# Optimization experiments

Measured on AMD Instinct MI355X. Metric: run time of the kernel, lower is better.

## Reference

```python
import jax, jax.numpy as jnp
import numpy as np

N = 50000      # total batched graph nodes (both ASTs of all examples)
E = 30000      # edges per edge type
T = 8          # num edge types (no master node, no sibling edges)
H = 128        # gnn hidden = change_vector_dim // 2
TAG = 32       # change-tag embed size
CONTENT = H - TAG
VOCAB = 20000  # rows of token/content encoding table
B = 64         # num examples
STEPS = (3, 3) # layer_time_steps


def setup_inputs() -> dict:
    key = jax.random.key(0)
    ks = jax.random.split(key, 22)
    s = 0.05
    inp = {}
    inp["node_content_ids"] = jax.random.randint(ks[0], (N,), 0, VOCAB)
    inp["node_tag_ids"] = jax.random.randint(ks[1], (N,), 0, 4)
    inp["edge_src"] = jax.random.randint(ks[2], (T, E), 0, N)
    inp["edge_tgt"] = jax.random.randint(ks[3], (T, E), 0, N)
    inp["node2example"] = jnp.sort(jax.random.randint(ks[4], (N,), 0, B))
    inp["content_table"] = jax.random.normal(ks[5], (VOCAB, CONTENT)) * s
    inp["tag_embedding"] = jax.random.normal(ks[6], (4, TAG)) * s
    inp["msg_W"] = jax.random.normal(ks[7], (2, T, H, H)) * s
    inp["msg_b"] = jax.random.normal(ks[8], (2, T, H)) * s
    inp["gru0_Wih"] = jax.random.normal(ks[9], (H, 3 * H)) * s
    inp["gru0_Whh"] = jax.random.normal(ks[10], (H, 3 * H)) * s
    inp["gru0_bih"] = jax.random.normal(ks[11], (3 * H,)) * s
    inp["gru0_bhh"] = jax.random.normal(ks[12], (3 * H,)) * s
    inp["gru1_Wih"] = jax.random.normal(ks[13], (2 * H, 3 * H)) * s  # layer 1 gets residual concat -> 2H input
    inp["gru1_Whh"] = jax.random.normal(ks[14], (H, 3 * H)) * s
    inp["gru1_bih"] = jax.random.normal(ks[15], (3 * H,)) * s
    inp["gru1_bhh"] = jax.random.normal(ks[16], (3 * H,)) * s
    inp["r1_w"] = jax.random.normal(ks[17], (H,)) * s
    inp["r1_b"] = jax.random.normal(ks[18], ()) * s
    inp["r2_w"] = jax.random.normal(ks[19], (H,)) * s
    inp["r2_b"] = jax.random.normal(ks[20], ()) * s
    return inp


def _gru(x, h, Wih, Whh, bih, bhh):
    # PyTorch GRUCell gate order: r, z, n
    gi = x @ Wih + bih
    gh = h @ Whh + bhh
    i_r, i_z, i_n = jnp.split(gi, 3, axis=-1)
    h_r, h_z, h_n = jnp.split(gh, 3, axis=-1)
    r = jax.nn.sigmoid(i_r + h_r)
    z = jax.nn.sigmoid(i_z + h_z)
    n = jnp.tanh(i_n + r * h_n)
    return (1.0 - z) * n + z * h


def reference(node_content_ids, node_tag_ids, edge_src, edge_tgt, node2example,
              content_table, tag_embedding, msg_W, msg_b,
              gru0_Wih, gru0_Whh, gru0_bih, gru0_bhh,
              gru1_Wih, gru1_Whh, gru1_bih, gru1_bhh,
              r1_w, r1_b, r2_w, r2_b):
    # init node embeddings: [token/content encoding || change-tag embedding] -> [N, H]
    init = jnp.concatenate([content_table[node_content_ids],
                            tag_embedding[node_tag_ids]], axis=-1)
    states = init
    layer_out = []
    for layer, steps in enumerate(STEPS):
        for _ in range(steps):
            src_states = states[edge_src]                                   # [T,E,H] gather
            msgs = jnp.einsum('teh,thd->ted', src_states, msg_W[layer]) \
                   + msg_b[layer][:, None, :]                               # per-edge-type linear
            agg = jnp.zeros_like(states).at[edge_tgt].add(msgs)             # scatter-add to targets
            if layer == 1:
                # residual_connections={1:[0]}: concat initial states with incoming messages
                x = jnp.concatenate([init, agg], axis=-1)
                states = _gru(x, states, gru1_Wih, gru1_Whh, gru1_bih, gru1_bhh)
            else:
                states = _gru(agg, states, gru0_Wih, gru0_Whh, gru0_bih, gru0_bhh)
        layer_out.append(states)
    s1, s2 = layer_out
    # gated scalar readout per layer, pooled per example, concatenated -> [B, 2H]
    g1 = jax.nn.sigmoid(s1 @ r1_w + r1_b)[:, None]
    g2 = jax.nn.sigmoid(s2 @ r2_w + r2_b)[:, None]
    pooled1 = jax.ops.segment_sum(g1 * s1, node2example, num_segments=B)
    pooled2 = jax.ops.segment_sum(g2 * s2, node2example, num_segments=B)
    return jnp.concatenate([pooled1, pooled2], axis=-1)
```

## Files before the change

kernel.cpp:

```cpp
#include <hip/hip_runtime.h>
#include <hip/hip_bf16.h>

#define NN 50000
#define NE 30000
#define NT 8
#define HH 128
#define NB 64
#define CONT 96
#define TPB 16
#define EDGES (NT * NE)
#define SBLK 512
#define SNB ((NN + SBLK - 1) / SBLK)
#define RCH 8
#define NTILE (NN / 16)
#define NPAIR ((NTILE + 1) / 2)
#define XB ((NPAIR + 3) / 4)
#define GGRID ((((XB + 7) / 8)) * 32)

typedef __attribute__((ext_vector_type(8))) short short8;
typedef __attribute__((ext_vector_type(4))) float f32x4;

__device__ __forceinline__ float sigm(float x) { return 1.f / (1.f + __expf(-x)); }
__device__ __forceinline__ float tanhf_fast(float x) {
  float e = __expf(2.f * x);
  return 1.f - 2.f / (e + 1.f);
}
__device__ __forceinline__ unsigned short bfbits(float x) {
  __hip_bfloat16 b = __float2bfloat16(x);
  return *(unsigned short*)&b;
}

__global__ __launch_bounds__(256) void init_kernel(
    const int* __restrict__ cid, const int* __restrict__ tg,
    const float* __restrict__ ctab, const float* __restrict__ ttab,
    __hip_bfloat16* __restrict__ sbf, __hip_bfloat16* __restrict__ ibf)
{
  int i = blockIdx.x * 256 + threadIdx.x;
  if (i >= NN * HH) return;
  int n = i >> 7, d = i & 127;
  float v;
  if (d < CONT) v = ctab[(size_t)cid[n] * CONT + d];
  else          v = ttab[(size_t)tg[n] * 32 + (d - CONT)];
  __hip_bfloat16 b = __float2bfloat16(v);
  sbf[i] = b;
  ibf[i] = b;
}

__global__ __launch_bounds__(256) void hist_kernel(
    const int* __restrict__ etgt, int* __restrict__ cnt)
{
  int i = blockIdx.x * 256 + threadIdx.x;
  if (i >= EDGES) return;
  atomicAdd(&cnt[etgt[i]], 1);
}

__global__ __launch_bounds__(SBLK) void scanA_kernel(
    const int* __restrict__ cnt, int* __restrict__ row_ptr, int* __restrict__ bsum)
{
  __shared__ int sm[SBLK];
  const int tid = threadIdx.x;
  const int i = blockIdx.x * SBLK + tid;
  int v = (i < NN) ? cnt[i] : 0;
  sm[tid] = v;
  __syncthreads();
  for (int off = 1; off < SBLK; off <<= 1) {
    int t = (tid >= off) ? sm[tid - off] : 0;
    __syncthreads();
    sm[tid] += t;
    __syncthreads();
  }
  if (i < NN) row_ptr[i] = sm[tid] - v;
  if (tid == SBLK - 1) bsum[blockIdx.x] = sm[tid];
}

__global__ __launch_bounds__(128) void scanB_kernel(
    const int* __restrict__ bsum, int* __restrict__ boff, int* __restrict__ row_ptr,
    const int* __restrict__ n2e, int* __restrict__ ebnd)
{
  __shared__ int sm[128];
  const int tid = threadIdx.x;
  int v = (tid < SNB) ? bsum[tid] : 0;
  sm[tid] = v;
  __syncthreads();
  for (int off = 1; off < 128; off <<= 1) {
    int t = (tid >= off) ? sm[tid - off] : 0;
    __syncthreads();
    sm[tid] += t;
    __syncthreads();
  }
  if (tid < SNB) boff[tid] = sm[tid] - v;
  if (tid == 127) row_ptr[NN] = sm[127];
  if (tid <= NB) {
    int lo = 0, hi = NN;
    while (lo < hi) { int mid = (lo + hi) >> 1; if (n2e[mid] < tid) lo = mid + 1; else hi = mid; }
    ebnd[tid] = lo;
  }
}

__global__ __launch_bounds__(SBLK) void scanC_kernel(
    int* __restrict__ row_ptr, int* __restrict__ cnt2, const int* __restrict__ boff)
{
  int i = blockIdx.x * SBLK + threadIdx.x;
  if (i >= NN) return;
  int r = row_ptr[i] + boff[blockIdx.x];
  row_ptr[i] = r;
  cnt2[i] = r;
}

__global__ __launch_bounds__(256) void scatter_kernel(
    const int* __restrict__ etgt, int* __restrict__ cnt2, int* __restrict__ perm)
{
  int i = blockIdx.x * 256 + threadIdx.x;
  if (i >= EDGES) return;
  perm[i] = atomicAdd(&cnt2[etgt[i]], 1);
}

__device__ __forceinline__ void gru_swz_one(
    const float* __restrict__ W, __hip_bfloat16* __restrict__ out, int KSL, int mode, int i)
{
  int j = i & 7, lane = (i >> 3) & 63, kk = (i >> 9) % KSL, nt = i / (KSL * 512);
  int hi = lane >> 4, lo = lane & 15;
  int p = kk * 32 + hi * 8 + j;
  int k;
  if (mode == 0)      k = p;
  else if (mode == 1) k = (p & 7) * 16 + (p >> 3);
  else                k = (p < 128) ? p : 128 + ((p - 128) & 7) * 16 + ((p - 128) >> 3);
  out[i] = __float2bfloat16(W[(size_t)k * 384 + nt * 16 + lo]);
}

__global__ __launch_bounds__(256) void wswz_all_kernel(
    const float* __restrict__ msgW, __hip_bfloat16* __restrict__ wswz,
    const float* __restrict__ g0Wih, __hip_bfloat16* __restrict__ w0ih,
    const float* __restrict__ g0Whh, __hip_bfloat16* __restrict__ w0hh,
    const float* __restrict__ g1Wih, __hip_bfloat16* __restrict__ w1ih,
    const float* __restrict__ g1Whh, __hip_bfloat16* __restrict__ w1hh)
{
  int i = blockIdx.x * 256 + threadIdx.x;
  if (i < 262144) {
    int j = i & 7, lane = (i >> 3) & 63, kk = (i >> 9) & 3, nt = (i >> 11) & 7, lt = i >> 14;
    int hi = lane >> 4, lo = lane & 15;
    int k = kk * 32 + hi * 8 + j;
    wswz[i] = __float2bfloat16(msgW[((size_t)lt * HH + k) * HH + nt * 16 + lo]);
    return;
  }
  i -= 262144;
  if (i < 49152)  { gru_swz_one(g0Wih, w0ih, 4, 1, i); return; }
  i -= 49152;
  if (i < 49152)  { gru_swz_one(g0Whh, w0hh, 4, 0, i); return; }
  i -= 49152;
  if (i < 98304)  { gru_swz_one(g1Wih, w1ih, 8, 2, i); return; }
  i -= 98304;
  if (i < 49152)  { gru_swz_one(g1Whh, w1hh, 4, 0, i); return; }
}

__global__ __launch_bounds__(256) void msg_mfma_kernel(
    const __hip_bfloat16* __restrict__ sbf, const int* __restrict__ esrc,
    const int* __restrict__ perm, const __hip_bfloat16* __restrict__ wswz,
    const float* __restrict__ ball, unsigned char* __restrict__ msgs8, int layer)
{
  __shared__ short8 Wl[8 * 4 * 64];
  const int t = blockIdx.y;
  {
    const float4* wg = (const float4*)(wswz + (size_t)(layer * NT + t) * 16384);
    float4* wl = (float4*)Wl;
    for (int i = threadIdx.x; i < 2048; i += 256) wl[i] = wg[i];
  }
  const int lane = threadIdx.x & 63;
  const int wv   = threadIdx.x >> 6;
  const int hi = lane >> 4, lo = lane & 15;
  float bias_v[8];
#pragma unroll
  for (int nt = 0; nt < 8; ++nt)
    bias_v[nt] = ball[(layer * NT + t) * HH + nt * 16 + lo];
  __syncthreads();

  const int tile_end = min((int)(blockIdx.x + 1) * TPB, NE / 16);
  for (int tile = blockIdx.x * TPB + wv; tile < tile_end; tile += 4) {
    const int e0 = tile * 16;
    const int src = esrc[t * NE + e0 + lo];
    const short* srow = (const short*)(sbf + (size_t)src * HH);
    short8 a[4];
#pragma unroll
    for (int kk = 0; kk < 4; ++kk)
      a[kk] = *(const short8*)(srow + kk * 32 + hi * 8);
    int slot[4];
#pragma unroll
    for (int r = 0; r < 4; ++r) slot[r] = perm[t * NE + e0 + hi * 4 + r];
    f32x4 acc[8];
#pragma unroll
    for (int nt = 0; nt < 8; ++nt) acc[nt] = (f32x4){0.f, 0.f, 0.f, 0.f};
#pragma unroll
    for (int nt = 0; nt < 8; ++nt)
#pragma unroll
      for (int kk = 0; kk < 4; ++kk)
        acc[nt] = __builtin_amdgcn_mfma_f32_16x16x32_bf16(
            a[kk], Wl[(nt * 4 + kk) * 64 + lane], acc[nt], 0, 0, 0);
#pragma unroll
    for (int r = 0; r < 4; ++r) {
      float m[8];
#pragma unroll
      for (int nt = 0; nt < 8; ++nt) m[nt] = acc[nt][r] + bias_v[nt];
      int u0 = 0, u1 = 0;
      u0 = __builtin_amdgcn_cvt_pk_fp8_f32(m[0], m[1], u0, false);
      u0 = __builtin_amdgcn_cvt_pk_fp8_f32(m[2], m[3], u0, true);
      u1 = __builtin_amdgcn_cvt_pk_fp8_f32(m[4], m[5], u1, false);
      u1 = __builtin_amdgcn_cvt_pk_fp8_f32(m[6], m[7], u1, true);
      uint2 st; st.x = (unsigned)u0; st.y = (unsigned)u1;
      *(uint2*)(msgs8 + (size_t)slot[r] * 128 + lo * 8) = st;
    }
  }
}

__global__ __launch_bounds__(256) void reduce_kernel(
    const unsigned char* __restrict__ msgs8, const int* __restrict__ row_ptr,
    __hip_bfloat16* __restrict__ agg)
{
  const int lane = threadIdx.x & 63;
  const int n = blockIdx.x * 4 + (threadIdx.x >> 6);
  if (n >= NN) return;
  const int b = row_ptr[n], e = row_ptr[n + 1];
  float a0 = 0.f, a1 = 0.f;
  for (int i = b; i < e; ++i) {
    unsigned int v = *(const unsigned short*)(msgs8 + (size_t)i * 128 + lane * 2);
    a0 += __builtin_amdgcn_cvt_f32_fp8(v, 0);
    a1 += __builtin_amdgcn_cvt_f32_fp8(v, 1);
  }
  unsigned int o = ((unsigned int)bfbits(a1) << 16) | bfbits(a0);
  *(unsigned int*)((short*)agg + (size_t)n * HH + lane * 2) = o;
}

__global__ __launch_bounds__(256) void giinit_kernel(
    const __hip_bfloat16* __restrict__ ibf,
    const __hip_bfloat16* __restrict__ Wih_s,
    const float* __restrict__ bih,
    __hip_bfloat16* __restrict__ gi)
{
  const int wg = blockIdx.x;
  const int xb = (wg >> 5) * 8 + (wg & 7);
  const int dtg = (wg >> 3) & 3;
  if (xb >= XB) return;

  __shared__ short8 BihL[2 * 3 * 4 * 64];
  {
    const short8* Bih_g = (const short8*)Wih_s;
    for (int i = threadIdx.x; i < 2 * 3 * 4 * 64; i += 256) {
      int lane_i = i & 63, kk = (i >> 6) & 3, g = ((i >> 6) >> 2) % 3, d2 = (i >> 6) / 12;
      BihL[i] = Bih_g[((size_t)(dtg * 2 + d2 + 8 * g) * 8 + kk) * 64 + lane_i];
    }
  }
  const int lane = threadIdx.x & 63;
  const int wv   = threadIdx.x >> 6;
  const int hi = lane >> 4, lo = lane & 15;
  float bv[2][3];
#pragma unroll
  for (int d2 = 0; d2 < 2; ++d2)
#pragma unroll
    for (int g = 0; g < 3; ++g)
      bv[d2][g] = bih[g * 128 + (dtg * 2 + d2) * 16 + lo];
  __syncthreads();

  const int pt = xb * 4 + wv;
  if (pt >= NPAIR) return;
  const int t0 = pt * 2;
  const bool two = (t0 + 1 < NTILE);

  short8 ax[2][4];
#pragma unroll
  for (int u = 0; u < 2; ++u) {
    const int nb = ((u && two) ? t0 + 1 : t0) * 16;
    const short* irow = (const short*)(ibf + (size_t)(nb + lo) * HH);
#pragma unroll
    for (int kk = 0; kk < 4; ++kk)
      ax[u][kk] = *(const short8*)(irow + kk * 32 + hi * 8);
  }

#pragma unroll
  for (int d2 = 0; d2 < 2; ++d2) {
    f32x4 aG[3][2];
#pragma unroll
    for (int g = 0; g < 3; ++g)
#pragma unroll
      for (int u = 0; u < 2; ++u) aG[g][u] = (f32x4){0.f, 0.f, 0.f, 0.f};
#pragma unroll
    for (int kk = 0; kk < 4; ++kk)
#pragma unroll
      for (int g = 0; g < 3; ++g) {
        short8 b = BihL[((d2 * 3 + g) * 4 + kk) * 64 + lane];
        aG[g][0] = __builtin_amdgcn_mfma_f32_16x16x32_bf16(ax[0][kk], b, aG[g][0], 0, 0, 0);
        aG[g][1] = __builtin_amdgcn_mfma_f32_16x16x32_bf16(ax[1][kk], b, aG[g][1], 0, 0, 0);
      }
    const int c = (dtg * 2 + d2) * 16 + lo;
    const int uend = two ? 2 : 1;
    for (int u = 0; u < uend; ++u) {
      const int nb = (t0 + u) * 16;
#pragma unroll
      for (int r = 0; r < 4; ++r) {
        const int node = nb + hi * 4 + r;
#pragma unroll
        for (int g = 0; g < 3; ++g)
          gi[(size_t)node * 384 + g * 128 + c] = __float2bfloat16(aG[g][u][r] + bv[d2][g]);
      }
    }
  }
}

template <int KSLT, int KOFF, bool GI>
__global__ __launch_bounds__(256) void gru_mfma_kernel(
    const __hip_bfloat16* __restrict__ agg,
    const __hip_bfloat16* __restrict__ gi,
    const __hip_bfloat16* __restrict__ hbf,
    const __hip_bfloat16* __restrict__ Wih_s,
    const __hip_bfloat16* __restrict__ Whh_s,
    const float* __restrict__ bih, const float* __restrict__ bhh,
    __hip_bfloat16* __restrict__ sbf_out)
{
  const int wg = blockIdx.x;
  const int xb = (wg >> 5) * 8 + (wg & 7);
  const int dtg = (wg >> 3) & 3;
  if (xb >= XB) return;

  __shared__ short8 BihL[2 * 3 * 4 * 64];
  {
    const short8* Bih_g = (const short8*)Wih_s;
    for (int i = threadIdx.x; i < 2 * 3 * 4 * 64; i += 256) {
      int lane_i = i & 63, kk = (i >> 6) & 3, g = ((i >> 6) >> 2) % 3, d2 = (i >> 6) / 12;
      BihL[i] = Bih_g[((size_t)(dtg * 2 + d2 + 8 * g) * KSLT + KOFF + kk) * 64 + lane_i];
    }
  }
  const int lane = threadIdx.x & 63;
  const int wv   = threadIdx.x >> 6;
  const int hi = lane >> 4, lo = lane & 15;
  float birv[2], bizv[2], binv[2], bhrv[2], bhzv[2], bhnv[2];
#pragma unroll
  for (int d2 = 0; d2 < 2; ++d2) {
    const int c = (dtg * 2 + d2) * 16 + lo;
    birv[d2] = bih[c]; bizv[d2] = bih[c + 128]; binv[d2] = bih[c + 256];
    bhrv[d2] = bhh[c]; bhzv[d2] = bhh[c + 128]; bhnv[d2] = bhh[c + 256];
  }
  __syncthreads();

  const int pt = xb * 4 + wv;
  if (pt >= NPAIR) return;
  const int t0 = pt * 2;
  const bool two = (t0 + 1 < NTILE);

  short8 ax[2][4], ah[2][4];
#pragma unroll
  for (int u = 0; u < 2; ++u) {
    const int nb = ((u && two) ? t0 + 1 : t0) * 16;
    const short* arow = (const short*)(agg + (size_t)(nb + lo) * HH);
    const short* hrow = (const short*)(hbf + (size_t)(nb + lo) * HH);
#pragma unroll
    for (int kk = 0; kk < 4; ++kk) {
      ax[u][kk] = *(const short8*)(arow + kk * 32 + hi * 8);
      ah[u][kk] = *(const short8*)(hrow + kk * 32 + hi * 8);
    }
  }

  const short8* __restrict__ Bhh_g = (const short8*)Whh_s;

#pragma unroll
  for (int d2 = 0; d2 < 2; ++d2) {
    const int dt = dtg * 2 + d2;
    f32x4 aR[2], aZ[2], aNi[2], aNh[2];
#pragma unroll
    for (int u = 0; u < 2; ++u) {
      aR[u] = (f32x4){0.f, 0.f, 0.f, 0.f};
      aZ[u] = (f32x4){0.f, 0.f, 0.f, 0.f};
      aNi[u] = (f32x4){0.f, 0.f, 0.f, 0.f};
      aNh[u] = (f32x4){0.f, 0.f, 0.f, 0.f};
    }
#pragma unroll
    for (int kk = 0; kk < 4; ++kk) {
      short8 br = BihL[((d2 * 3 + 0) * 4 + kk) * 64 + lane];
      short8 bz = BihL[((d2 * 3 + 1) * 4 + kk) * 64 + lane];
      short8 bn = BihL[((d2 * 3 + 2) * 4 + kk) * 64 + lane];
#pragma unroll
      for (int u = 0; u < 2; ++u) {
        aR[u]  = __builtin_amdgcn_mfma_f32_16x16x32_bf16(ax[u][kk], br, aR[u], 0, 0, 0);
        aZ[u]  = __builtin_amdgcn_mfma_f32_16x16x32_bf16(ax[u][kk], bz, aZ[u], 0, 0, 0);
        aNi[u] = __builtin_amdgcn_mfma_f32_16x16x32_bf16(ax[u][kk], bn, aNi[u], 0, 0, 0);
      }
    }
#pragma unroll
    for (int kk = 0; kk < 4; ++kk) {
      short8 br = Bhh_g[((size_t)(dt     ) * 4 + kk) * 64 + lane];
      short8 bz = Bhh_g[((size_t)(dt +  8) * 4 + kk) * 64 + lane];
      short8 bn = Bhh_g[((size_t)(dt + 16) * 4 + kk) * 64 + lane];
#pragma unroll
      for (int u = 0; u < 2; ++u) {
        aR[u]  = __builtin_amdgcn_mfma_f32_16x16x32_bf16(ah[u][kk], br, aR[u], 0, 0, 0);
        aZ[u]  = __builtin_amdgcn_mfma_f32_16x16x32_bf16(ah[u][kk], bz, aZ[u], 0, 0, 0);
        aNh[u] = __builtin_amdgcn_mfma_f32_16x16x32_bf16(ah[u][kk], bn, aNh[u], 0, 0, 0);
      }
    }
    const int c = dt * 16 + lo;
    const int uend = two ? 2 : 1;
    for (int u = 0; u < uend; ++u) {
      const int nb = (t0 + u) * 16;
#pragma unroll
      for (int r = 0; r < 4; ++r) {
        const int node = nb + hi * 4 + r;
        float gr, gz, gn;
        if (GI) {
          gr = __bfloat162float(gi[(size_t)node * 384 + c]);
          gz = __bfloat162float(gi[(size_t)node * 384 + 128 + c]);
          gn = __bfloat162float(gi[(size_t)node * 384 + 256 + c]);
        } else {
          gr = birv[d2]; gz = bizv[d2]; gn = binv[d2];
        }
        const float rg = sigm(aR[u][r] + gr + bhrv[d2]);
        const float zg = sigm(aZ[u][r] + gz + bhzv[d2]);
        const float ng = tanhf_fast(aNi[u][r] + gn + rg * (aNh[u][r] + bhnv[d2]));
        const float hc = __bfloat162float(hbf[(size_t)node * HH + c]);
        sbf_out[(size_t)node * HH + c] = __float2bfloat16((1.f - zg) * ng + zg * hc);
      }
    }
  }
}

__global__ __launch_bounds__(256) void readout_kernel(
    const __hip_bfloat16* __restrict__ sbf, const int* __restrict__ ebnd,
    const float* __restrict__ rw, const float* __restrict__ rb,
    float* __restrict__ out, int coff)
{
  __shared__ float sm[4][128];
  const int ex = blockIdx.x / RCH, ch = blockIdx.x % RCH;
  const int s = ebnd[ex], e = ebnd[ex + 1];
  const int lane = threadIdx.x & 63;
  const int wv   = threadIdx.x >> 6;
  const float w0 = rw[2 * lane], w1 = rw[2 * lane + 1], rbv = rb[0];
  float a0 = 0.f, a1 = 0.f;
  for (int n = s + ch * 4 + wv; n < e; n += 4 * RCH) {
    unsigned int v = *(const unsigned int*)((const short*)sbf + (size_t)n * HH + lane * 2);
    const float s0 = __uint_as_float(v << 16);
    const float s1 = __uint_as_float(v & 0xffff0000u);
    float p = s0 * w0 + s1 * w1;
#pragma unroll
    for (int o = 32; o; o >>= 1) p += __shfl_xor(p, o, 64);
    const float g = sigm(p + rbv);
    a0 += g * s0;
    a1 += g * s1;
  }
  sm[wv][2 * lane] = a0;
  sm[wv][2 * lane + 1] = a1;
  __syncthreads();
  if (wv == 0) {
    const int c0 = 2 * lane, c1 = 2 * lane + 1;
    float v0 = sm[0][c0] + sm[1][c0] + sm[2][c0] + sm[3][c0];
    float v1 = sm[0][c1] + sm[1][c1] + sm[2][c1] + sm[3][c1];
    atomicAdd(&out[(size_t)ex * (2 * HH) + coff + c0], v0);
    atomicAdd(&out[(size_t)ex * (2 * HH) + coff + c1], v1);
  }
}

extern "C" void kernel_launch(void* const* d_in, const int* in_sizes, int n_in,
                              void* d_out, int out_size, void* d_ws, size_t ws_size,
                              hipStream_t stream)
{
  const int*   cid   = (const int*)d_in[0];
  const int*   tg    = (const int*)d_in[1];
  const int*   esrc  = (const int*)d_in[2];
  const int*   etgt  = (const int*)d_in[3];
  const int*   n2e   = (const int*)d_in[4];
  const float* ctab  = (const float*)d_in[5];
  const float* ttab  = (const float*)d_in[6];
  const float* msgW  = (const float*)d_in[7];
  const float* msgb  = (const float*)d_in[8];
  const float* g0Wih = (const float*)d_in[9];
  const float* g0Whh = (const float*)d_in[10];
  const float* g0bih = (const float*)d_in[11];
  const float* g0bhh = (const float*)d_in[12];
  const float* g1Wih = (const float*)d_in[13];
  const float* g1Whh = (const float*)d_in[14];
  const float* g1bih = (const float*)d_in[15];
  const float* g1bhh = (const float*)d_in[16];
  const float* r1w   = (const float*)d_in[17];
  const float* r1b   = (const float*)d_in[18];
  const float* r2w   = (const float*)d_in[19];
  const float* r2b   = (const float*)d_in[20];

  float* out = (float*)d_out;
  __hip_bfloat16* sb0  = (__hip_bfloat16*)d_ws;
  __hip_bfloat16* sb1  = sb0 + (size_t)NN * HH;
  __hip_bfloat16* ibf  = sb1 + (size_t)NN * HH;
  __hip_bfloat16* agg  = ibf + (size_t)NN * HH;
  __hip_bfloat16* gi   = agg + (size_t)NN * HH;
  unsigned char*  msgs8 = (unsigned char*)(gi + (size_t)NN * 384);
  __hip_bfloat16* wswz = (__hip_bfloat16*)(msgs8 + (size_t)EDGES * 128);
  __hip_bfloat16* w0ih = wswz + 262144;
  __hip_bfloat16* w0hh = w0ih + 24 * 4 * 512;
  __hip_bfloat16* w1ih = w0hh + 24 * 4 * 512;
  __hip_bfloat16* w1hh = w1ih + 24 * 8 * 512;
  int* row_ptr = (int*)(w1hh + 24 * 4 * 512);
  int* cnt     = row_ptr + NN + 1;
  int* cnt2    = cnt + NN;
  int* perm    = cnt2 + NN;
  int* bsum    = perm + EDGES;
  int* boff    = bsum + SNB;
  int* ebnd    = boff + SNB;

  hipMemsetAsync(d_out, 0, (size_t)NB * 2 * HH * sizeof(float), stream);
  hipMemsetAsync(cnt, 0, (size_t)NN * sizeof(int), stream);
  const int eblocks = (EDGES + 255) / 256;
  hist_kernel<<<eblocks, 256, 0, stream>>>(etgt, cnt);
  scanA_kernel<<<SNB, SBLK, 0, stream>>>(cnt, row_ptr, bsum);
  scanB_kernel<<<1, 128, 0, stream>>>(bsum, boff, row_ptr, n2e, ebnd);
  scanC_kernel<<<SNB, SBLK, 0, stream>>>(row_ptr, cnt2, boff);
  scatter_kernel<<<eblocks, 256, 0, stream>>>(etgt, cnt2, perm);

  wswz_all_kernel<<<507904 / 256, 256, 0, stream>>>(msgW, wswz, g0Wih, w0ih, g0Whh, w0hh,
                                                    g1Wih, w1ih, g1Whh, w1hh);
  init_kernel<<<(NN * HH + 255) / 256, 256, 0, stream>>>(cid, tg, ctab, ttab, sb0, ibf);
  giinit_kernel<<<GGRID, 256, 0, stream>>>(ibf, w1ih, g1bih, gi);

  dim3 mgrid((NE / 16 + TPB - 1) / TPB, NT);
  const int rblocks = (NN + 3) / 4;
  __hip_bfloat16* cur = sb0;
  __hip_bfloat16* nxt = sb1;
  for (int s = 0; s < 3; ++s) {
    msg_mfma_kernel<<<mgrid, 256, 0, stream>>>(cur, esrc, perm, wswz, msgb, msgs8, 0);
    reduce_kernel<<<rblocks, 256, 0, stream>>>(msgs8, row_ptr, agg);
    gru_mfma_kernel<4, 0, false><<<GGRID, 256, 0, stream>>>(agg, nullptr, cur, w0ih, w0hh,
                                                            g0bih, g0bhh, nxt);
    __hip_bfloat16* t = cur; cur = nxt; nxt = t;
  }
  readout_kernel<<<NB * RCH, 256, 0, stream>>>(cur, ebnd, r1w, r1b, out, 0);

  for (int s = 0; s < 3; ++s) {
    msg_mfma_kernel<<<mgrid, 256, 0, stream>>>(cur, esrc, perm, wswz, msgb, msgs8, 1);
    reduce_kernel<<<rblocks, 256, 0, stream>>>(msgs8, row_ptr, agg);
    gru_mfma_kernel<8, 4, true><<<GGRID, 256, 0, stream>>>(agg, gi, cur, w1ih, w1hh,
                                                           g1bih, g1bhh, nxt);
    __hip_bfloat16* t = cur; cur = nxt; nxt = t;
  }
  readout_kernel<<<NB * RCH, 256, 0, stream>>>(cur, ebnd, r2w, r2b, out, HH);
}
```

Baseline: 621.2 us.

## Store GRU gate inputs and hidden state in MFMA fragment layout, stage Whh in LDS

Adds a second copy of the hidden state stored in MFMA accumulator-fragment order. The GRU epilogue can then read the previous hidden value with one 8-byte vector load per lane instead of strided scalar bf16 loads. The precomputed layer-1 gate inputs (gi) are likewise stored in fragment order and read as short4 vectors, and the Whh weights are staged in LDS alongside Wih. The cost is an extra fragment-layout write per GRU step and in init, more workspace, and doubled LDS per block, which may reduce occupancy.

```diff
diff --git a/kernel.cpp b/kernel.cpp
--- a/kernel.cpp
+++ b/kernel.cpp
@@ -18,6 +18,7 @@
 #define GGRID ((((XB + 7) / 8)) * 32)
 
 typedef __attribute__((ext_vector_type(8))) short short8;
+typedef __attribute__((ext_vector_type(4))) short short4v;
 typedef __attribute__((ext_vector_type(4))) float f32x4;
 
 __device__ __forceinline__ float sigm(float x) { return 1.f / (1.f + __expf(-x)); }
@@ -29,11 +30,14 @@
   __hip_bfloat16 b = __float2bfloat16(x);
   return *(unsigned short*)&b;
 }
+__device__ __forceinline__ float bf2f(unsigned short u) {
+  return __uint_as_float(((unsigned int)u) << 16);
+}
 
 __global__ __launch_bounds__(256) void init_kernel(
     const int* __restrict__ cid, const int* __restrict__ tg,
     const float* __restrict__ ctab, const float* __restrict__ ttab,
-    __hip_bfloat16* __restrict__ sbf, __hip_bfloat16* __restrict__ ibf)
+    __hip_bfloat16* __restrict__ sbf, short* __restrict__ sfrag)
 {
   int i = blockIdx.x * 256 + threadIdx.x;
   if (i >= NN * HH) return;
@@ -41,9 +45,11 @@
   float v;
   if (d < CONT) v = ctab[(size_t)cid[n] * CONT + d];
   else          v = ttab[(size_t)tg[n] * 32 + (d - CONT)];
-  __hip_bfloat16 b = __float2bfloat16(v);
-  sbf[i] = b;
-  ibf[i] = b;
+  unsigned short b = bfbits(v);
+  *(unsigned short*)&sbf[i] = b;
+  int tile = n >> 4, rr = n & 15, hi = rr >> 2, r = rr & 3;
+  int dt = d >> 4, lo = d & 15;
+  sfrag[(((size_t)tile * 8 + dt) * 64 + hi * 16 + lo) * 4 + r] = (short)b;
 }
 
 __global__ __launch_bounds__(256) void hist_kernel(
@@ -233,7 +239,7 @@
     const __hip_bfloat16* __restrict__ ibf,
     const __hip_bfloat16* __restrict__ Wih_s,
     const float* __restrict__ bih,
-    __hip_bfloat16* __restrict__ gi)
+    short* __restrict__ gi)
 {
   const int wg = blockIdx.x;
   const int xb = (wg >> 5) * 8 + (wg & 7);
@@ -276,6 +282,7 @@
 
 #pragma unroll
   for (int d2 = 0; d2 < 2; ++d2) {
+    const int dt = dtg * 2 + d2;
     f32x4 aG[3][2];
 #pragma unroll
     for (int g = 0; g < 3; ++g)
@@ -289,16 +296,16 @@
         aG[g][0] = __builtin_amdgcn_mfma_f32_16x16x32_bf16(ax[0][kk], b, aG[g][0], 0, 0, 0);
         aG[g][1] = __builtin_amdgcn_mfma_f32_16x16x32_bf16(ax[1][kk], b, aG[g][1], 0, 0, 0);
       }
-    const int c = (dtg * 2 + d2) * 16 + lo;
     const int uend = two ? 2 : 1;
     for (int u = 0; u < uend; ++u) {
-      const int nb = (t0 + u) * 16;
-#pragma unroll
-      for (int r = 0; r < 4; ++r) {
-        const int node = nb + hi * 4 + r;
-#pragma unroll
-        for (int g = 0; g < 3; ++g)
-          gi[(size_t)node * 384 + g * 128 + c] = __float2bfloat16(aG[g][u][r] + bv[d2][g]);
+      const int tile = t0 + u;
+#pragma unroll
+      for (int g = 0; g < 3; ++g) {
+        short4v st;
+#pragma unroll
+        for (int r = 0; r < 4; ++r)
+          ((unsigned short*)&st)[r] = bfbits(aG[g][u][r] + bv[d2][g]);
+        *(short4v*)&gi[((((size_t)tile * 8 + dt) * 3 + g) * 64 + lane) * 4] = st;
       }
     }
   }
@@ -307,12 +314,14 @@
 template <int KSLT, int KOFF, bool GI>
 __global__ __launch_bounds__(256) void gru_mfma_kernel(
     const __hip_bfloat16* __restrict__ agg,
-    const __hip_bfloat16* __restrict__ gi,
+    const short* __restrict__ gi,
     const __hip_bfloat16* __restrict__ hbf,
+    const short* __restrict__ hfrag,
     const __hip_bfloat16* __restrict__ Wih_s,
     const __hip_bfloat16* __restrict__ Whh_s,
     const float* __restrict__ bih, const float* __restrict__ bhh,
-    __hip_bfloat16* __restrict__ sbf_out)
+    __hip_bfloat16* __restrict__ sbf_out,
+    short* __restrict__ sfrag_out)
 {
   const int wg = blockIdx.x;
   const int xb = (wg >> 5) * 8 + (wg & 7);
@@ -320,11 +329,14 @@
   if (xb >= XB) return;
 
   __shared__ short8 BihL[2 * 3 * 4 * 64];
+  __shared__ short8 BhhL[2 * 3 * 4 * 64];
   {
     const short8* Bih_g = (const short8*)Wih_s;
+    const short8* Bhh_g = (const short8*)Whh_s;
     for (int i = threadIdx.x; i < 2 * 3 * 4 * 64; i += 256) {
       int lane_i = i & 63, kk = (i >> 6) & 3, g = ((i >> 6) >> 2) % 3, d2 = (i >> 6) / 12;
       BihL[i] = Bih_g[((size_t)(dtg * 2 + d2 + 8 * g) * KSLT + KOFF + kk) * 64 + lane_i];
+      BhhL[i] = Bhh_g[((size_t)(dtg * 2 + d2 + 8 * g) * 4 + kk) * 64 + lane_i];
     }
   }
   const int lane = threadIdx.x & 63;
@@ -356,8 +368,6 @@
       ah[u][kk] = *(const short8*)(hrow + kk * 32 + hi * 8);
     }
   }
-
-  const short8* __restrict__ Bhh_g = (const short8*)Whh_s;
 
 #pragma unroll
   for (int d2 = 0; d2 < 2; ++d2) {
@@ -384,9 +394,9 @@
     }
 #pragma unroll
     for (int kk = 0; kk < 4; ++kk) {
-      short8 br = Bhh_g[((size_t)(dt     ) * 4 + kk) * 64 + lane];
-      short8 bz = Bhh_g[((size_t)(dt +  8) * 4 + kk) * 64 + lane];
-      short8 bn = Bhh_g[((size_t)(dt + 16) * 4 + kk) * 64 + lane];
+      short8 br = BhhL[((d2 * 3 + 0) * 4 + kk) * 64 + lane];
+      short8 bz = BhhL[((d2 * 3 + 1) * 4 + kk) * 64 + lane];
+      short8 bn = BhhL[((d2 * 3 + 2) * 4 + kk) * 64 + lane];
 #pragma unroll
       for (int u = 0; u < 2; ++u) {
         aR[u]  = __builtin_amdgcn_mfma_f32_16x16x32_bf16(ah[u][kk], br, aR[u], 0, 0, 0);
@@ -397,24 +407,36 @@
     const int c = dt * 16 + lo;
     const int uend = two ? 2 : 1;
     for (int u = 0; u < uend; ++u) {
-      const int nb = (t0 + u) * 16;
+      const int tile = t0 + u;
+      const int nb = tile * 16;
+      short4v hv = *(const short4v*)&hfrag[(((size_t)tile * 8 + dt) * 64 + lane) * 4];
+      short4v gv0, gv1, gv2;
+      if (GI) {
+        gv0 = *(const short4v*)&gi[((((size_t)tile * 8 + dt) * 3 + 0) * 64 + lane) * 4];
+        gv1 = *(const short4v*)&gi[((((size_t)tile * 8 + dt) * 3 + 1) * 64 + lane) * 4];
+        gv2 = *(const short4v*)&gi[((((size_t)tile * 8 + dt) * 3 + 2) * 64 + lane) * 4];
+      }
+      short4v hnv;
 #pragma unroll
       for (int r = 0; r < 4; ++r) {
         const int node = nb + hi * 4 + r;
         float gr, gz, gn;
         if (GI) {
-          gr = __bfloat162float(gi[(size_t)node * 384 + c]);
-          gz = __bfloat162float(gi[(size_t)node * 384 + 128 + c]);
-          gn = __bfloat162float(gi[(size_t)node * 384 + 256 + c]);
+          gr = bf2f(((unsigned short*)&gv0)[r]);
+          gz = bf2f(((unsigned short*)&gv1)[r]);
+          gn = bf2f(((unsigned short*)&gv2)[r]);
         } else {
           gr = birv[d2]; gz = bizv[d2]; gn = binv[d2];
         }
         const float rg = sigm(aR[u][r] + gr + bhrv[d2]);
         const float zg = sigm(aZ[u][r] + gz + bhzv[d2]);
         const float ng = tanhf_fast(aNi[u][r] + gn + rg * (aNh[u][r] + bhnv[d2]));
-        const float hc = __bfloat162float(hbf[(size_t)node * HH + c]);
-        sbf_out[(size_t)node * HH + c] = __float2bfloat16((1.f - zg) * ng + zg * hc);
+        const float hc = bf2f(((unsigned short*)&hv)[r]);
+        const unsigned short hb = bfbits((1.f - zg) * ng + zg * hc);
+        ((unsigned short*)&hnv)[r] = hb;
+        *(unsigned short*)&sbf_out[(size_t)node * HH + c] = hb;
       }
+      *(short4v*)&sfrag_out[(((size_t)tile * 8 + dt) * 64 + lane) * 4] = hnv;
     }
   }
 }
@@ -483,10 +505,11 @@
   float* out = (float*)d_out;
   __hip_bfloat16* sb0  = (__hip_bfloat16*)d_ws;
   __hip_bfloat16* sb1  = sb0 + (size_t)NN * HH;
-  __hip_bfloat16* ibf  = sb1 + (size_t)NN * HH;
-  __hip_bfloat16* agg  = ibf + (size_t)NN * HH;
-  __hip_bfloat16* gi   = agg + (size_t)NN * HH;
-  unsigned char*  msgs8 = (unsigned char*)(gi + (size_t)NN * 384);
+  short* sf0 = (short*)(sb1 + (size_t)NN * HH);
+  short* sf1 = sf0 + (size_t)NN * HH;
+  __hip_bfloat16* agg  = (__hip_bfloat16*)(sf1 + (size_t)NN * HH);
+  short* gi = (short*)(agg + (size_t)NN * HH);
+  unsigned char* msgs8 = (unsigned char*)(gi + (size_t)NN * 384);
   __hip_bfloat16* wswz = (__hip_bfloat16*)(msgs8 + (size_t)EDGES * 128);
   __hip_bfloat16* w0ih = wswz + 262144;
   __hip_bfloat16* w0hh = w0ih + 24 * 4 * 512;
@@ -511,28 +534,32 @@
 
   wswz_all_kernel<<<507904 / 256, 256, 0, stream>>>(msgW, wswz, g0Wih, w0ih, g0Whh, w0hh,
                                                     g1Wih, w1ih, g1Whh, w1hh);
-  init_kernel<<<(NN * HH + 255) / 256, 256, 0, stream>>>(cid, tg, ctab, ttab, sb0, ibf);
-  giinit_kernel<<<GGRID, 256, 0, stream>>>(ibf, w1ih, g1bih, gi);
+  init_kernel<<<(NN * HH + 255) / 256, 256, 0, stream>>>(cid, tg, ctab, ttab, sb0, sf0);
+  giinit_kernel<<<GGRID, 256, 0, stream>>>(sb0, w1ih, g1bih, gi);
 
   dim3 mgrid((NE / 16 + TPB - 1) / TPB, NT);
   const int rblocks = (NN + 3) / 4;
-  __hip_bfloat16* cur = sb0;
-  __hip_bfloat16* nxt = sb1;
+  __hip_bfloat16* cur = sb0;  __hip_bfloat16* nxt = sb1;
+  short* fcur = sf0;          short* fnxt = sf1;
   for (int s = 0; s < 3; ++s) {
     msg_mfma_kernel<<<mgrid, 256, 0, stream>>>(cur, esrc, perm, wswz, msgb, msgs8, 0);
     reduce_kernel<<<rblocks, 256, 0, stream>>>(msgs8, row_ptr, agg);
-    gru_mfma_kernel<4, 0, false><<<GGRID, 256, 0, stream>>>(agg, nullptr, cur, w0ih, w0hh,
-                                                            g0bih, g0bhh, nxt);
+    gru_mfma_kernel<4, 0, false><<<GGRID, 256, 0, stream>>>(agg, nullptr, cur, fcur,
+                                                            w0ih, w0hh, g0bih, g0bhh,
+                                                            nxt, fnxt);
     __hip_bfloat16* t = cur; cur = nxt; nxt = t;
+    short* ft = fcur; fcur = fnxt; fnxt = ft;
   }
   readout_kernel<<<NB * RCH, 256, 0, stream>>>(cur, ebnd, r1w, r1b, out, 0);
 
   for (int s = 0; s < 3; ++s) {
     msg_mfma_kernel<<<mgrid, 256, 0, stream>>>(cur, esrc, perm, wswz, msgb, msgs8, 1);
     reduce_kernel<<<rblocks, 256, 0, stream>>>(msgs8, row_ptr, agg);
-    gru_mfma_kernel<8, 4, true><<<GGRID, 256, 0, stream>>>(agg, gi, cur, w1ih, w1hh,
-                                                           g1bih, g1bhh, nxt);
+    gru_mfma_kernel<8, 4, true><<<GGRID, 256, 0, stream>>>(agg, gi, cur, fcur,
+                                                           w1ih, w1hh, g1bih, g1bhh,
+                                                           nxt, fnxt);
     __hip_bfloat16* t = cur; cur = nxt; nxt = t;
+    short* ft = fcur; fcur = fnxt; fnxt = ft;
   }
   readout_kernel<<<NB * RCH, 256, 0, stream>>>(cur, ebnd, r2w, r2b, out, HH);
 }
```

After: 604.5 us (median of 2 runs). -2.7%, faster.
